# Performance work log

Hardware: AMD Instinct MI355X
Metric: run time of the kernel (lower is better)

Reference implementation:

```python
import jax, jax.numpy as jnp
import numpy as np

EPS = 1e-8
EPS12 = 1e-12
TAU = 0.2
IOU_THRESHOLD = 0.5
NEG_INF = -1e9

N, C = 8192, 1024
HID, FGD, CLSD = 256, 64, 128


def setup_inputs() -> dict:
    key = jax.random.key(0)
    ks = jax.random.split(key, 16)
    roi_feats = jax.random.normal(ks[0], (N, C), dtype=jnp.float32)
    # labels in {-1 (ignore), 0 (bg), 1..20 (classes)}
    labels = jax.random.randint(ks[1], (N,), 0, 21, dtype=jnp.int64) - 1
    ious = jax.random.uniform(ks[2], (N,), dtype=jnp.float32)
    s = 0.02
    w1f = jax.random.normal(ks[3], (HID, C), dtype=jnp.float32) * s
    b1f = jnp.zeros((HID,), dtype=jnp.float32)
    w2f = jax.random.normal(ks[4], (FGD, HID), dtype=jnp.float32) * s
    b2f = jnp.zeros((FGD,), dtype=jnp.float32)
    w1c = jax.random.normal(ks[5], (HID, C), dtype=jnp.float32) * s
    b1c = jnp.zeros((HID,), dtype=jnp.float32)
    w2c = jax.random.normal(ks[6], (CLSD, HID), dtype=jnp.float32) * s
    b2c = jnp.zeros((CLSD,), dtype=jnp.float32)
    return {"roi_feats": roi_feats, "labels": labels, "ious": ious,
            "w1f": w1f, "b1f": b1f, "w2f": w2f, "b2f": b2f,
            "w1c": w1c, "b1c": b1c, "w2c": w2c, "b2c": b2c}


def _project_normalize(x, w1, b1, w2, b2):
    h = jax.nn.relu(x @ w1.T + b1)
    z = h @ w2.T + b2
    nrm = jnp.linalg.norm(z, axis=1, keepdims=True)  # F.normalize: z / max(||z||, eps)
    return z / jnp.maximum(nrm, EPS)


def _fg_bg_loss(z_fg, fg_mask, ignore_mask, iou_weight):
    n = z_fg.shape[0]
    anchor = fg_mask & ~ignore_mask
    eye = jnp.eye(n, dtype=bool)
    # pos_mask[i,j] = fg_mask[j] & ~ignore[j], self excluded
    pos = (fg_mask & ~ignore_mask)[None, :] & ~eye  # [N,N]
    sim = (z_fg @ z_fg.T) / TAU
    sim_exp = jnp.exp(sim) * (~eye).astype(sim.dtype)
    denom = sim_exp.sum(axis=1)  # [N]
    numer = jnp.sum(jnp.exp(sim) * pos.astype(sim.dtype), axis=1)  # [N]
    n_pos = pos.sum(axis=1)
    loss_i = -jnp.log((numer + EPS) / (denom + EPS))
    valid = anchor & (n_pos > 0)
    w = iou_weight
    num = jnp.sum(jnp.where(valid, loss_i * w, 0.0))
    den = jnp.sum(jnp.where(valid, w, 0.0)) + EPS
    return num / den


def _class_supcon_loss(z_cls, labels, fg_mask, ignore_mask, iou_weight):
    n = z_cls.shape[0]
    anchor = fg_mask & ~ignore_mask
    eye = jnp.eye(n, dtype=bool)
    valid_den = ~eye & ~ignore_mask[None, :]  # [N,N]
    # pos[i,j]: same label, j not ignored, labels[j] != 0, j != i, j valid
    pos = (labels[None, :] == labels[:, None]) & ~ignore_mask[None, :] & (labels[None, :] != 0)
    pos = pos & ~eye & valid_den
    sim = (z_cls @ z_cls.T) / TAU
    logits = jnp.where(valid_den, sim, NEG_INF)
    denom_log = jax.nn.logsumexp(logits, axis=1)  # [N]
    n_pos = pos.sum(axis=1)
    sum_pos = jnp.sum(jnp.where(pos, sim, 0.0), axis=1)
    n_pos_safe = jnp.maximum(n_pos, 1).astype(sim.dtype)
    loss_i = -(sum_pos - n_pos.astype(sim.dtype) * denom_log) / n_pos_safe
    valid = anchor & (n_pos > 0) & valid_den.any(axis=1)
    w = iou_weight
    num = jnp.sum(jnp.where(valid, loss_i * w, 0.0))
    den = jnp.sum(jnp.where(valid, w, 0.0)) + EPS12
    return num / den


def reference(roi_feats, labels, ious, w1f, b1f, w2f, b2f, w1c, b1c, w2c, b2c):
    z_fg = _project_normalize(roi_feats, w1f, b1f, w2f, b2f)
    z_cls = _project_normalize(roi_feats, w1c, b1c, w2c, b2c)
    ignore_mask = labels == -1
    bg_mask = (labels == 0) & ~ignore_mask
    fg_mask = (labels > 0) & ~ignore_mask
    iou_weight = jnp.where(ious > IOU_THRESHOLD, ious, 0.0)
    loss_fg_bg = _fg_bg_loss(z_fg, fg_mask, ignore_mask, iou_weight)
    loss_supcon = _class_supcon_loss(z_cls, labels, fg_mask, ignore_mask, iou_weight)
    # loss_weights = (1.0, 1.0); stacked as [loss_fg_bg, loss_supcon]
    return jnp.stack([loss_fg_bg * 1.0, loss_supcon * 1.0])
```

## Files before the change

### kernel.cpp

```cpp
#include <hip/hip_runtime.h>
#include <hip/hip_bf16.h>
#include <math.h>

#define N_ROI 8192
#define C_IN  1024
#define HIDD  256
#define FGD   64
#define CLSD  128
#define INV_TAU 5.0f
#define SCALE_LOG2E 7.2134752f
#define LN2F 0.69314718f

using frag_ab = __attribute__((ext_vector_type(8))) short;
using f32x16  = __attribute__((ext_vector_type(16))) float;

static __device__ __forceinline__ short f32_to_bf16_bits(float f) {
  unsigned u = __builtin_bit_cast(unsigned, f);
  u = (u + 0x7FFFu + ((u >> 16) & 1u)) >> 16;
  return (short)u;
}
static __device__ __forceinline__ float bf16_bits_to_f32(short b) {
  unsigned u = ((unsigned)(unsigned short)b) << 16;
  return __builtin_bit_cast(float, u);
}
static __device__ __forceinline__ float fast_exp2(float x) {
#if __has_builtin(__builtin_amdgcn_exp2f)
  return __builtin_amdgcn_exp2f(x);
#else
  return exp2f(x);
#endif
}
static __device__ __forceinline__ void async_copy16(const void* g, void* l) {
  __builtin_amdgcn_global_load_lds(
      (const __attribute__((address_space(1))) unsigned int*)g,
      (__attribute__((address_space(3))) unsigned int*)l, 16, 0, 0);
}

__global__ __launch_bounds__(256) void pack_zero_kernel(
    const float* __restrict__ w1f, const float* __restrict__ w1c,
    const float* __restrict__ w2f, const float* __restrict__ w2c,
    short* __restrict__ W1pf, short* __restrict__ W1pc,
    short* __restrict__ W2pf, short* __restrict__ W2pc,
    float* __restrict__ accum, int* __restrict__ cnt) {
  int b = blockIdx.x;
  if (b == 280) {
    int t = threadIdx.x;
    if (t < 8) accum[t] = 0.f;
    if (t < 24) cnt[t] = 0;
    return;
  }
  const float* src; short* dst; int Ksh; int b0;
  if (b < 128)      { src = w1f; dst = W1pf; Ksh = 10; b0 = 0; }
  else if (b < 256) { src = w1c; dst = W1pc; Ksh = 10; b0 = 128; }
  else if (b < 264) { src = w2f; dst = W2pf; Ksh = 8;  b0 = 256; }
  else              { src = w2c; dst = W2pc; Ksh = 8;  b0 = 264; }
  int K = 1 << Ksh;
  int f = (b - b0) * 256 + threadIdx.x;
  int r = f >> (Ksh - 3);
  int c0 = (f & ((K >> 3) - 1)) << 3;
  float4 v0 = *(const float4*)(src + (size_t)r * K + c0);
  float4 v1 = *(const float4*)(src + (size_t)r * K + c0 + 4);
  union { short s[8]; uint4 v; } o;
  o.s[0] = f32_to_bf16_bits(v0.x); o.s[1] = f32_to_bf16_bits(v0.y);
  o.s[2] = f32_to_bf16_bits(v0.z); o.s[3] = f32_to_bf16_bits(v0.w);
  o.s[4] = f32_to_bf16_bits(v1.x); o.s[5] = f32_to_bf16_bits(v1.y);
  o.s[6] = f32_to_bf16_bits(v1.z); o.s[7] = f32_to_bf16_bits(v1.w);
  ((uint4*)dst)[(size_t)((r >> 5) * (K >> 4) + (c0 >> 4)) * 64 +
                ((c0 >> 3) & 1) * 32 + (r & 31)] = o.v;
}

template<int D>
__device__ __forceinline__ void gemm2_from_lds(
    const short* __restrict__ T2,
    const short* __restrict__ W2p, const float* __restrict__ b2,
    short* __restrict__ Zr, float* __restrict__ tii,
    short* __restrict__ T, int gt) {
  int lane = threadIdx.x & 63;
  const frag_ab* Wv = (const frag_ab*)W2p;
  constexpr int NT = D / 32;
  frag_ab a[16];
  #pragma unroll
  for (int kc = 0; kc < 16; ++kc)
    a[kc] = *(const frag_ab*)&T2[(lane & 31) * 264 + kc * 16 + (lane >> 5) * 8];
  f32x16 acc[NT];
  #pragma unroll
  for (int j = 0; j < NT; ++j)
    #pragma unroll
    for (int q = 0; q < 16; ++q) acc[j][q] = 0.f;
  #pragma unroll
  for (int kc = 0; kc < 16; ++kc)
    #pragma unroll
    for (int j = 0; j < NT; ++j)
      acc[j] = __builtin_amdgcn_mfma_f32_32x32x16_bf16(a[kc], Wv[(j * 16 + kc) * 64 + lane], acc[j], 0, 0, 0);
  int c = lane & 31, h = lane >> 5;
  float bb[NT];
  #pragma unroll
  for (int j = 0; j < NT; ++j) bb[j] = b2[j * 32 + c];
  float s1[16];
  #pragma unroll
  for (int r = 0; r < 16; ++r) {
    s1[r] = 0.f;
    #pragma unroll
    for (int j = 0; j < NT; ++j) {
      float v = acc[j][r] + bb[j];
      s1[r] += v * v;
    }
  }
  #pragma unroll
  for (int r = 0; r < 16; ++r)
    #pragma unroll
    for (int m = 1; m < 32; m <<= 1) s1[r] += __shfl_xor(s1[r], m);
  float s2[16];
  #pragma unroll
  for (int r = 0; r < 16; ++r) s2[r] = 0.f;
  #pragma unroll
  for (int j = 0; j < NT; ++j) {
    int cl = j * 32 + c;
    #pragma unroll
    for (int g = 0; g < 4; ++g) {
      short q0, q1, q2, q3;
      #pragma unroll
      for (int e = 0; e < 4; ++e) {
        int r = g * 4 + e;
        float sc = 1.f / fmaxf(sqrtf(s1[r]), 1e-8f);
        short qb = f32_to_bf16_bits((acc[j][r] + bb[j]) * sc);
        float zf = bf16_bits_to_f32(qb);
        s2[r] += zf * zf;
        if (e == 0) q0 = qb; else if (e == 1) q1 = qb; else if (e == 2) q2 = qb; else q3 = qb;
      }
      *(short4*)&T[cl * 36 + 4 * h + 8 * g] = make_short4(q0, q1, q2, q3);
    }
  }
  #pragma unroll
  for (int r = 0; r < 16; ++r)
    #pragma unroll
    for (int m = 1; m < 32; m <<= 1) s2[r] += __shfl_xor(s2[r], m);
  if (c == 0) {
    #pragma unroll
    for (int r = 0; r < 16; ++r)
      tii[gt * 32 + (r & 3) + 8 * (r >> 2) + 4 * h] = s2[r];
  }
  uint4* Zv = (uint4*)Zr;
  #pragma unroll
  for (int k = 0; k < D / 16; ++k) {
    int c0 = (2 * k + h) * 8;
    union { short s[8]; uint4 u; } o;
    #pragma unroll
    for (int e = 0; e < 8; ++e) o.s[e] = T[(c0 + e) * 36 + c];
    Zv[(size_t)(gt * (D / 16) + k) * 64 + h * 32 + c] = o.u;
  }
}

__global__ __launch_bounds__(256) void fused_mlp_kernel(
    const float* __restrict__ X,
    const short* __restrict__ W1pf, const short* __restrict__ W1pc,
    const float* __restrict__ b1f, const float* __restrict__ b1c,
    const short* __restrict__ W2pf, const short* __restrict__ W2pc,
    const float* __restrict__ b2f, const float* __restrict__ b2c,
    short* __restrict__ Zrf, short* __restrict__ Zrc,
    float* __restrict__ tiif, float* __restrict__ tiic,
    const int* __restrict__ labels,
    float* __restrict__ Sfg, float* __restrict__ Pfg,
    float* __restrict__ Scls, float* __restrict__ SPc,
    float* __restrict__ pfv, float* __restrict__ nimv,
    float* __restrict__ ljmv, int* __restrict__ cnt) {
  __shared__ short stageA[2][1024];
  __shared__ short T2[32 * 264];
  __shared__ short Tw[128 * 36];
  int tid = threadIdx.x, lane = tid & 63, wv = tid >> 6;
  int Mb = blockIdx.x, head = blockIdx.y;

  if (head == 0 && tid < 32) {
    int i = Mb * 32 + tid;
    Sfg[i] = 0.f; Pfg[i] = 0.f; Scls[i] = 0.f; SPc[i] = 0.f;
    int l = labels[i];
    pfv[i]  = (l > 0)  ? 1.f : 0.f;
    nimv[i] = (l != -1) ? 1.f : 0.f;
    ljmv[i] = (l > 0)  ? (float)l : -7.f;
    int b = l + 1; if (b < 0) b = 0; if (b > 21) b = 21;
    atomicAdd(&cnt[b], 1);
  }

  const short* Wp = head ? W1pc : W1pf;
  const float* b1 = head ? b1c  : b1f;
  const uint4* Wv4 = (const uint4*)Wp;
  int arow = tid >> 3;
  int ac4  = tid & 7;
  const float* Xp = X + (size_t)(Mb * 32 + arow) * C_IN + ac4 * 4;
  int aslot = ((ac4 >> 2) * 64 + ((ac4 >> 1) & 1) * 32 + arow) * 8 + (ac4 & 1) * 4;

  float4 av[4];
  frag_ab breg[3][4];
  f32x16 acc[2];
  #pragma unroll
  for (int nt = 0; nt < 2; ++nt)
    #pragma unroll
    for (int q = 0; q < 16; ++q) acc[nt][q] = 0.f;

  auto loadA = [&](int c, int s) { av[s] = *(const float4*)(Xp + c * 32); };
  auto loadB = [&](int c, int s) {
    #pragma unroll
    for (int kci = 0; kci < 2; ++kci)
      #pragma unroll
      for (int nt = 0; nt < 2; ++nt)
        breg[s][kci * 2 + nt] =
            *(const frag_ab*)&Wv4[(size_t)((wv * 2 + nt) * 64 + c * 2 + kci) * 64 + lane];
  };
  auto storeA = [&](int buf, int s) {
    *(short4*)&stageA[buf][aslot] =
        make_short4(f32_to_bf16_bits(av[s].x), f32_to_bf16_bits(av[s].y),
                    f32_to_bf16_bits(av[s].z), f32_to_bf16_bits(av[s].w));
  };
  auto domfma = [&](int buf, int bank) {
    frag_ab a0 = *(const frag_ab*)&stageA[buf][(0 * 64 + lane) * 8];
    frag_ab a1 = *(const frag_ab*)&stageA[buf][(1 * 64 + lane) * 8];
    #pragma unroll
    for (int nt = 0; nt < 2; ++nt)
      acc[nt] = __builtin_amdgcn_mfma_f32_32x32x16_bf16(a0, breg[bank][nt], acc[nt], 0, 0, 0);
    #pragma unroll
    for (int nt = 0; nt < 2; ++nt)
      acc[nt] = __builtin_amdgcn_mfma_f32_32x32x16_bf16(a1, breg[bank][2 + nt], acc[nt], 0, 0, 0);
  };
  auto lds_barrier = [&]() {
    asm volatile("s_waitcnt lgkmcnt(0)" ::: "memory");
    __builtin_amdgcn_s_barrier();
    __builtin_amdgcn_sched_barrier(0);
  };

  loadA(0, 0); loadA(1, 1); loadA(2, 2); loadA(3, 3);
  loadB(0, 0); loadB(1, 1);
  storeA(0, 0);
  lds_barrier();

  #pragma unroll
  for (int c = 0; c < 32; ++c) {
    if (c + 2 < 32) loadB(c + 2, (c + 2) % 3);
    if (c + 4 < 32) loadA(c + 4, (c + 4) & 3);
    domfma(c & 1, c % 3);
    if (c + 1 < 32) {
      storeA((c + 1) & 1, (c + 1) & 3);
      lds_barrier();
    }
  }
  {
    int cl31 = lane & 31, h = lane >> 5;
    #pragma unroll
    for (int nt = 0; nt < 2; ++nt) {
      int gc = wv * 64 + nt * 32 + cl31;
      float bb = b1[gc];
      #pragma unroll
      for (int q = 0; q < 16; ++q) {
        int row = (q & 3) + 8 * (q >> 2) + 4 * h;
        float x = fmaxf(acc[nt][q] + bb, 0.f);
        T2[row * 264 + gc] = f32_to_bf16_bits(x);
      }
    }
  }
  __syncthreads();

  if (wv == 0) {
    if (head == 0)
      gemm2_from_lds<FGD>(T2, W2pf, b2f, Zrf, tiif, Tw, Mb);
    else
      gemm2_from_lds<CLSD>(T2, W2pc, b2c, Zrc, tiic, Tw, Mb);
  }
}

template<int D, int MODE, int NJT>
__device__ __forceinline__ void loss_body(
    const short* __restrict__ Zr, const int* __restrict__ labels,
    const float* __restrict__ pfv, const float* __restrict__ nimv,
    const float* __restrict__ ljmv,
    float* __restrict__ Sg, float* __restrict__ Pg,
    short* __restrict__ smem) {
  constexpr int KC = D / 16;
  constexpr int JP = (MODE == 0) ? 2 : 1;
  constexpr int NIT = NJT / JP;
  constexpr int BUF_SH = 4096;
  int tid = threadIdx.x, lane = tid & 63, wv = tid >> 6;
  int itile = (blockIdx.x >> 1) * 8 + wv;
  int jt0 = blockIdx.y * NJT;
  int jlane = lane & 31;
  const frag_ab* Zrv = (const frag_ab*)Zr;

  frag_ab a[KC];
  #pragma unroll
  for (int kc = 0; kc < KC; ++kc) {
    frag_ab t = Zrv[(itile * KC + kc) * 64 + lane];
    #pragma unroll
    for (int e = 0; e < 8; ++e)
      t[e] = f32_to_bf16_bits(bf16_bits_to_f32(t[e]) * SCALE_LOG2E);
    a[kc] = t;
  }
  float limf[16];
  if (MODE == 1) {
    #pragma unroll
    for (int r = 0; r < 16; ++r) {
      int row = (r & 3) + 8 * (r >> 2) + 4 * (lane >> 5);
      limf[r] = (float)labels[itile * 32 + row];
    }
  }
  __builtin_amdgcn_sched_barrier(0);
  asm volatile("s_waitcnt vmcnt(0)" ::: "memory");
  __builtin_amdgcn_sched_barrier(0);

  short* b0 = smem;
  short* b1 = smem + BUF_SH;
  short* b2 = smem + 2 * BUF_SH;
  float* maskf = (float*)(smem + 3 * BUF_SH);

  if (MODE == 0) {
    async_copy16(pfv + jt0 * 32 + (size_t)(tid & 127) * 4,
                 maskf + (wv & 1) * 256);
  } else {
    const float* msrc = ((wv & 2) == 0) ? nimv : ljmv;
    float* mdst = maskf + ((wv & 2) ? 512 : 0) + (wv & 1) * 256;
    async_copy16(msrc + jt0 * 32 + (size_t)(tid & 127) * 4, mdst);
  }

  auto STAGE = [&](short* dst, int it) {
    const short* src = Zr + (size_t)(jt0 + it * JP) * KC * 512 / JP * JP;
    async_copy16(src + (size_t)tid * 8, dst + wv * 512);
  };

  STAGE(b0, 0); STAGE(b1, 1);

  float Ssum[16] = {}, Psum[16] = {};

  #pragma unroll 1
  for (int t = 0; t < NIT; ++t) {
    if (t < NIT - 1) asm volatile("s_waitcnt vmcnt(1)" ::: "memory");
    else             asm volatile("s_waitcnt vmcnt(0)" ::: "memory");
    __builtin_amdgcn_s_barrier();
    __builtin_amdgcn_sched_barrier(0);
    if (t + 2 < NIT) STAGE(b2, t + 2);

    if (MODE == 0) {
      float pf0 = maskf[t * 64 + jlane];
      float pf1 = maskf[t * 64 + 32 + jlane];
      f32x16 acc0, acc1;
      #pragma unroll
      for (int q = 0; q < 16; ++q) { acc0[q] = 0.f; acc1[q] = 0.f; }
      __builtin_amdgcn_s_setprio(1);
      #pragma unroll
      for (int kc = 0; kc < KC; ++kc) {
        frag_ab bb0 = *(const frag_ab*)&b0[(kc * 64 + lane) * 8];
        frag_ab bb1 = *(const frag_ab*)&b0[((KC + kc) * 64 + lane) * 8];
        acc0 = __builtin_amdgcn_mfma_f32_32x32x16_bf16(a[kc], bb0, acc0, 0, 0, 0);
        acc1 = __builtin_amdgcn_mfma_f32_32x32x16_bf16(a[kc], bb1, acc1, 0, 0, 0);
      }
      __builtin_amdgcn_s_setprio(0);
      #pragma unroll
      for (int rr = 0; rr < 16; ++rr) {
        float e0 = fast_exp2(acc0[rr]);
        float e1 = fast_exp2(acc1[rr]);
        Ssum[rr] += e0 + e1;
        Psum[rr] = fmaf(pf0, e0, fmaf(pf1, e1, Psum[rr]));
      }
    } else {
      float nim = maskf[t * 32 + jlane];
      float ljm = maskf[512 + t * 32 + jlane];
      f32x16 acc;
      #pragma unroll
      for (int q = 0; q < 16; ++q) acc[q] = 0.f;
      __builtin_amdgcn_s_setprio(1);
      #pragma unroll
      for (int kc = 0; kc < KC; ++kc) {
        frag_ab b = *(const frag_ab*)&b0[(kc * 64 + lane) * 8];
        acc = __builtin_amdgcn_mfma_f32_32x32x16_bf16(a[kc], b, acc, 0, 0, 0);
      }
      __builtin_amdgcn_s_setprio(0);
      #pragma unroll
      for (int rr = 0; rr < 16; ++rr) {
        float e = fast_exp2(acc[rr]);
        Ssum[rr] = fmaf(nim, e, Ssum[rr]);
        Psum[rr] += (limf[rr] == ljm) ? acc[rr] : 0.f;
      }
    }
    short* tmp = b0; b0 = b1; b1 = b2; b2 = tmp;
  }

  #pragma unroll
  for (int r = 0; r < 16; ++r) {
    float s = Ssum[r], p = Psum[r];
    #pragma unroll
    for (int m = 1; m < 32; m <<= 1) { s += __shfl_xor(s, m); p += __shfl_xor(p, m); }
    if ((lane & 31) == 0) {
      if (MODE == 1) p *= LN2F;
      int row = (r & 3) + 8 * (r >> 2) + 4 * (lane >> 5);
      atomicAdd(&Sg[itile * 32 + row], s);
      atomicAdd(&Pg[itile * 32 + row], p);
    }
  }
}

__global__ __launch_bounds__(512, 2) void loss_kernel(
    const short* __restrict__ Zrf, const short* __restrict__ Zrc,
    const int* __restrict__ labels,
    const float* __restrict__ pfv, const float* __restrict__ nimv,
    const float* __restrict__ ljmv,
    float* __restrict__ Sfg, float* __restrict__ Pfg,
    float* __restrict__ Scls, float* __restrict__ SPc) {
  __shared__ short smem[3 * 4096 + 2048];
  if ((blockIdx.x & 1) == 0)
    loss_body<FGD, 0, 16>(Zrf, labels, pfv, nimv, ljmv, Sfg, Pfg, smem);
  else
    loss_body<CLSD, 1, 16>(Zrc, labels, pfv, nimv, ljmv, Scls, SPc, smem);
}

__global__ __launch_bounds__(256) void finalize_kernel(
    const float* __restrict__ Sfg, const float* __restrict__ Pfg,
    const float* __restrict__ Scls, const float* __restrict__ SPc,
    const float* __restrict__ tiif, const float* __restrict__ tiic,
    const int* __restrict__ labels, const float* __restrict__ ious,
    int* __restrict__ cnt, float* __restrict__ accum, float* __restrict__ out) {
  int i = blockIdx.x * 256 + threadIdx.x;
  int l = labels[i];
  float iv = ious[i];
  float w = (iv > 0.5f) ? iv : 0.f;
  int cntP = 0;
  #pragma unroll
  for (int b = 2; b <= 21; ++b) cntP += cnt[b];
  int cntNI = N_ROI - cnt[0];
  bool Pi = (l > 0);
  float numF = 0.f, denF = 0.f, numC = 0.f, denC = 0.f;
  float eF = __expf(INV_TAU * tiif[i]);
  float Sf = Sfg[i] - eF;
  float Pf = Pfg[i] - (Pi ? eF : 0.f);
  int nposF = cntP - (Pi ? 1 : 0);
  if (Pi && nposF > 0) {
    float lossF = logf((Sf + 1e-8f) / (Pf + 1e-8f));
    numF = lossF * w; denF = w;
  }
  float tC = INV_TAU * tiic[i];
  float eC = __expf(tC);
  float Sc = Scls[i] - ((l != -1) ? eC : 0.f);
  float SP = SPc[i] - (Pi ? tC : 0.f);
  int nposC = Pi ? (cnt[l + 1] - 1) : 0;
  bool anyv = (cntNI - ((l != -1) ? 1 : 0)) > 0;
  if (Pi && nposC > 0 && anyv) {
    float lse = logf(Sc);
    float lossC = -(SP - (float)nposC * lse) / fmaxf((float)nposC, 1.f);
    numC = lossC * w; denC = w;
  }
  float v0 = numF, v1 = denF, v2 = numC, v3 = denC;
  #pragma unroll
  for (int m = 1; m < 64; m <<= 1) {
    v0 += __shfl_xor(v0, m); v1 += __shfl_xor(v1, m);
    v2 += __shfl_xor(v2, m); v3 += __shfl_xor(v3, m);
  }
  __shared__ float red[4][4];
  int lane = threadIdx.x & 63, wid = threadIdx.x >> 6;
  if (lane == 0) { red[wid][0]=v0; red[wid][1]=v1; red[wid][2]=v2; red[wid][3]=v3; }
  __syncthreads();
  if (threadIdx.x == 0) {
    float s0=0,s1=0,s2=0,s3=0;
    for (int q = 0; q < 4; ++q) { s0+=red[q][0]; s1+=red[q][1]; s2+=red[q][2]; s3+=red[q][3]; }
    atomicAdd(&accum[0], s0); atomicAdd(&accum[1], s1);
    atomicAdd(&accum[2], s2); atomicAdd(&accum[3], s3);
    __threadfence();
    int t = atomicAdd(&cnt[22], 1);
    if (t == 31) {
      __threadfence();
      out[0] = accum[0] / (accum[1] + 1e-8f);
      out[1] = accum[2] / (accum[3] + 1e-12f);
    }
  }
}

extern "C" void kernel_launch(void* const* d_in, const int* in_sizes, int n_in,
                              void* d_out, int out_size, void* d_ws, size_t ws_size,
                              hipStream_t stream) {
  const float* X    = (const float*)d_in[0];
  const int*  labels= (const int*)d_in[1];
  const float* ious = (const float*)d_in[2];
  const float* w1f  = (const float*)d_in[3];
  const float* b1f  = (const float*)d_in[4];
  const float* w2f  = (const float*)d_in[5];
  const float* b2f  = (const float*)d_in[6];
  const float* w1c  = (const float*)d_in[7];
  const float* b1c  = (const float*)d_in[8];
  const float* w2c  = (const float*)d_in[9];
  const float* b2c  = (const float*)d_in[10];
  float* out = (float*)d_out;

  char* w = (char*)d_ws;
  short* W1pf = (short*)w;            w += 524288;
  short* W1pc = (short*)w;            w += 524288;
  short* W2pf = (short*)w;            w += 32768;
  short* W2pc = (short*)w;            w += 65536;
  short* Zrf  = (short*)w;            w += 1048576;
  short* Zrc  = (short*)w;            w += 2097152;
  float* Sfg  = (float*)w;            w += 32768;
  float* Pfg  = (float*)w;            w += 32768;
  float* Scls = (float*)w;            w += 32768;
  float* SPc  = (float*)w;            w += 32768;
  float* tiif = (float*)w;            w += 32768;
  float* tiic = (float*)w;            w += 32768;
  float* pfv  = (float*)w;            w += 32768;
  float* nimv = (float*)w;            w += 32768;
  float* ljmv = (float*)w;            w += 32768;
  float* accum= (float*)w;            w += 32;
  int*   cnt  = (int*)w;              w += 96;

  pack_zero_kernel<<<281, 256, 0, stream>>>(w1f, w1c, w2f, w2c,
                                            W1pf, W1pc, W2pf, W2pc, accum, cnt);

  fused_mlp_kernel<<<dim3(256, 2), 256, 0, stream>>>(X, W1pf, W1pc, b1f, b1c,
                                            W2pf, W2pc, b2f, b2c,
                                            Zrf, Zrc, tiif, tiic,
                                            labels, Sfg, Pfg, Scls, SPc,
                                            pfv, nimv, ljmv, cnt);

  loss_kernel<<<dim3(64, 16), 512, 0, stream>>>(Zrf, Zrc, labels, pfv, nimv, ljmv,
                                                Sfg, Pfg, Scls, SPc);

  finalize_kernel<<<N_ROI/256, 256, 0, stream>>>(Sfg, Pfg, Scls, SPc, tiif, tiic,
                                                 labels, ious, cnt, accum, out);
}
```

Measured before the change: 184.9 us.

## Replace per-pair positive-sim sum with per-class embedding sums and dot product

The same-class positive similarity sum is rewritten algebraically as z_i dotted with the sum of z_j over class l_i. A new kernel builds the 20 per-class sums, and the finalize kernel computes the dot product, so the class loss loop no longer needs label compares or a second accumulator. The class branch now processes two j-tiles per iteration like the fg branch, with larger LDS buffers. This adds a kernel launch and atomics, and the dot product uses unscaled bf16 Z, which may shift precision slightly.

```diff
diff --git a/kernel.cpp b/kernel.cpp
--- a/kernel.cpp
+++ b/kernel.cpp
@@ -41,12 +41,14 @@
     const float* __restrict__ w2f, const float* __restrict__ w2c,
     short* __restrict__ W1pf, short* __restrict__ W1pc,
     short* __restrict__ W2pf, short* __restrict__ W2pc,
-    float* __restrict__ accum, int* __restrict__ cnt) {
+    float* __restrict__ accum, int* __restrict__ cnt,
+    float* __restrict__ Vc) {
   int b = blockIdx.x;
   if (b == 280) {
     int t = threadIdx.x;
     if (t < 8) accum[t] = 0.f;
     if (t < 24) cnt[t] = 0;
+    for (int q = t; q < 2560; q += 256) Vc[q] = 0.f;
     return;
   }
   const float* src; short* dst; int Ksh; int b0;
@@ -161,9 +163,9 @@
     float* __restrict__ tiif, float* __restrict__ tiic,
     const int* __restrict__ labels,
     float* __restrict__ Sfg, float* __restrict__ Pfg,
-    float* __restrict__ Scls, float* __restrict__ SPc,
+    float* __restrict__ Scls,
     float* __restrict__ pfv, float* __restrict__ nimv,
-    float* __restrict__ ljmv, int* __restrict__ cnt) {
+    int* __restrict__ cnt) {
   __shared__ short stageA[2][1024];
   __shared__ short T2[32 * 264];
   __shared__ short Tw[128 * 36];
@@ -172,11 +174,10 @@
 
   if (head == 0 && tid < 32) {
     int i = Mb * 32 + tid;
-    Sfg[i] = 0.f; Pfg[i] = 0.f; Scls[i] = 0.f; SPc[i] = 0.f;
+    Sfg[i] = 0.f; Pfg[i] = 0.f; Scls[i] = 0.f;
     int l = labels[i];
     pfv[i]  = (l > 0)  ? 1.f : 0.f;
     nimv[i] = (l != -1) ? 1.f : 0.f;
-    ljmv[i] = (l > 0)  ? (float)l : -7.f;
     int b = l + 1; if (b < 0) b = 0; if (b > 21) b = 21;
     atomicAdd(&cnt[b], 1);
   }
@@ -266,17 +267,48 @@
   }
 }
 
+__global__ __launch_bounds__(128) void classsum_kernel(
+    const short* __restrict__ Zrc, const int* __restrict__ labels,
+    float* __restrict__ Vc) {
+  __shared__ int lidx[512];
+  __shared__ int lcnt;
+  int c = blockIdx.x + 1;
+  int d = threadIdx.x;
+  int j0 = blockIdx.y * 512;
+  if (d == 0) lcnt = 0;
+  __syncthreads();
+  #pragma unroll
+  for (int u = 0; u < 4; ++u) {
+    int row = j0 + u * 128 + d;
+    if (labels[row] == c) {
+      int k = atomicAdd(&lcnt, 1);
+      lidx[k] = row;
+    }
+  }
+  __syncthreads();
+  int n = lcnt;
+  int kc = d >> 4, h = (d >> 3) & 1, e = d & 7;
+  float acc = 0.f;
+  for (int k = 0; k < n; ++k) {
+    int row = lidx[k];
+    int jt = row >> 5, r = row & 31;
+    acc += bf16_bits_to_f32(
+        Zrc[((size_t)((jt * 8 + kc) * 64 + h * 32 + r)) * 8 + e]);
+  }
+  atomicAdd(&Vc[(c - 1) * 128 + d], acc);
+}
+
 template<int D, int MODE, int NJT>
 __device__ __forceinline__ void loss_body(
-    const short* __restrict__ Zr, const int* __restrict__ labels,
-    const float* __restrict__ pfv, const float* __restrict__ nimv,
-    const float* __restrict__ ljmv,
+    const short* __restrict__ Zr,
+    const float* __restrict__ maskv,
     float* __restrict__ Sg, float* __restrict__ Pg,
     short* __restrict__ smem) {
   constexpr int KC = D / 16;
-  constexpr int JP = (MODE == 0) ? 2 : 1;
+  constexpr int JP = 2;
   constexpr int NIT = NJT / JP;
-  constexpr int BUF_SH = 4096;
+  constexpr int BUFQ = JP * KC * 512;
+  constexpr int LD = BUFQ / 4096;
   int tid = threadIdx.x, lane = tid & 63, wv = tid >> 6;
   int itile = (blockIdx.x >> 1) * 8 + wv;
   int jt0 = blockIdx.y * NJT;
@@ -292,35 +324,23 @@
       t[e] = f32_to_bf16_bits(bf16_bits_to_f32(t[e]) * SCALE_LOG2E);
     a[kc] = t;
   }
-  float limf[16];
-  if (MODE == 1) {
-    #pragma unroll
-    for (int r = 0; r < 16; ++r) {
-      int row = (r & 3) + 8 * (r >> 2) + 4 * (lane >> 5);
-      limf[r] = (float)labels[itile * 32 + row];
-    }
-  }
   __builtin_amdgcn_sched_barrier(0);
   asm volatile("s_waitcnt vmcnt(0)" ::: "memory");
   __builtin_amdgcn_sched_barrier(0);
 
   short* b0 = smem;
-  short* b1 = smem + BUF_SH;
-  short* b2 = smem + 2 * BUF_SH;
-  float* maskf = (float*)(smem + 3 * BUF_SH);
-
-  if (MODE == 0) {
-    async_copy16(pfv + jt0 * 32 + (size_t)(tid & 127) * 4,
-                 maskf + (wv & 1) * 256);
-  } else {
-    const float* msrc = ((wv & 2) == 0) ? nimv : ljmv;
-    float* mdst = maskf + ((wv & 2) ? 512 : 0) + (wv & 1) * 256;
-    async_copy16(msrc + jt0 * 32 + (size_t)(tid & 127) * 4, mdst);
-  }
+  short* b1 = smem + BUFQ;
+  short* b2 = smem + 2 * BUFQ;
+  float* maskf = (float*)(smem + 3 * BUFQ);
+
+  async_copy16(maskv + jt0 * 32 + (size_t)(tid & 127) * 4,
+               maskf + (wv & 1) * 256);
 
   auto STAGE = [&](short* dst, int it) {
-    const short* src = Zr + (size_t)(jt0 + it * JP) * KC * 512 / JP * JP;
-    async_copy16(src + (size_t)tid * 8, dst + wv * 512);
+    const short* src = Zr + (size_t)(jt0 + it * JP) * KC * 512;
+    #pragma unroll
+    for (int u = 0; u < LD; ++u)
+      async_copy16(src + (size_t)(u * 512 + tid) * 8, dst + u * 4096 + wv * 512);
   };
 
   STAGE(b0, 0); STAGE(b1, 1);
@@ -329,52 +349,37 @@
 
   #pragma unroll 1
   for (int t = 0; t < NIT; ++t) {
-    if (t < NIT - 1) asm volatile("s_waitcnt vmcnt(1)" ::: "memory");
-    else             asm volatile("s_waitcnt vmcnt(0)" ::: "memory");
+    if (t < NIT - 1) {
+      if constexpr (LD == 1) asm volatile("s_waitcnt vmcnt(1)" ::: "memory");
+      else                   asm volatile("s_waitcnt vmcnt(2)" ::: "memory");
+    } else {
+      asm volatile("s_waitcnt vmcnt(0)" ::: "memory");
+    }
     __builtin_amdgcn_s_barrier();
     __builtin_amdgcn_sched_barrier(0);
     if (t + 2 < NIT) STAGE(b2, t + 2);
 
-    if (MODE == 0) {
-      float pf0 = maskf[t * 64 + jlane];
-      float pf1 = maskf[t * 64 + 32 + jlane];
-      f32x16 acc0, acc1;
-      #pragma unroll
-      for (int q = 0; q < 16; ++q) { acc0[q] = 0.f; acc1[q] = 0.f; }
-      __builtin_amdgcn_s_setprio(1);
-      #pragma unroll
-      for (int kc = 0; kc < KC; ++kc) {
-        frag_ab bb0 = *(const frag_ab*)&b0[(kc * 64 + lane) * 8];
-        frag_ab bb1 = *(const frag_ab*)&b0[((KC + kc) * 64 + lane) * 8];
-        acc0 = __builtin_amdgcn_mfma_f32_32x32x16_bf16(a[kc], bb0, acc0, 0, 0, 0);
-        acc1 = __builtin_amdgcn_mfma_f32_32x32x16_bf16(a[kc], bb1, acc1, 0, 0, 0);
-      }
-      __builtin_amdgcn_s_setprio(0);
-      #pragma unroll
-      for (int rr = 0; rr < 16; ++rr) {
-        float e0 = fast_exp2(acc0[rr]);
-        float e1 = fast_exp2(acc1[rr]);
+    float m0 = maskf[t * 64 + jlane];
+    float m1 = maskf[t * 64 + 32 + jlane];
+    f32x16 acc0, acc1;
+    #pragma unroll
+    for (int q = 0; q < 16; ++q) { acc0[q] = 0.f; acc1[q] = 0.f; }
+    #pragma unroll
+    for (int kc = 0; kc < KC; ++kc) {
+      frag_ab bb0 = *(const frag_ab*)&b0[(kc * 64 + lane) * 8];
+      frag_ab bb1 = *(const frag_ab*)&b0[((KC + kc) * 64 + lane) * 8];
+      acc0 = __builtin_amdgcn_mfma_f32_32x32x16_bf16(a[kc], bb0, acc0, 0, 0, 0);
+      acc1 = __builtin_amdgcn_mfma_f32_32x32x16_bf16(a[kc], bb1, acc1, 0, 0, 0);
+    }
+    #pragma unroll
+    for (int rr = 0; rr < 16; ++rr) {
+      float e0 = fast_exp2(acc0[rr]);
+      float e1 = fast_exp2(acc1[rr]);
+      if (MODE == 0) {
         Ssum[rr] += e0 + e1;
-        Psum[rr] = fmaf(pf0, e0, fmaf(pf1, e1, Psum[rr]));
-      }
-    } else {
-      float nim = maskf[t * 32 + jlane];
-      float ljm = maskf[512 + t * 32 + jlane];
-      f32x16 acc;
-      #pragma unroll
-      for (int q = 0; q < 16; ++q) acc[q] = 0.f;
-      __builtin_amdgcn_s_setprio(1);
-      #pragma unroll
-      for (int kc = 0; kc < KC; ++kc) {
-        frag_ab b = *(const frag_ab*)&b0[(kc * 64 + lane) * 8];
-        acc = __builtin_amdgcn_mfma_f32_32x32x16_bf16(a[kc], b, acc, 0, 0, 0);
-      }
-      __builtin_amdgcn_s_setprio(0);
-      #pragma unroll
-      for (int rr = 0; rr < 16; ++rr) {
-        float e = fast_exp2(acc[rr]);
-        Ssum[rr] = fmaf(nim, e, Ssum[rr]);
-        Psum[rr] += (limf[rr] == ljm) ? acc[rr] : 0.f;
+        Psum[rr] = fmaf(m0, e0, fmaf(m1, e1, Psum[rr]));
+      } else {
+        Ssum[rr] = fmaf(m1, e1, fmaf(m0, e0, Ssum[rr]));
       }
     }
     short* tmp = b0; b0 = b1; b1 = b2; b2 = tmp;
@@ -384,33 +389,34 @@
   for (int r = 0; r < 16; ++r) {
     float s = Ssum[r], p = Psum[r];
     #pragma unroll
-    for (int m = 1; m < 32; m <<= 1) { s += __shfl_xor(s, m); p += __shfl_xor(p, m); }
+    for (int m = 1; m < 32; m <<= 1) {
+      s += __shfl_xor(s, m);
+      if (MODE == 0) p += __shfl_xor(p, m);
+    }
     if ((lane & 31) == 0) {
-      if (MODE == 1) p *= LN2F;
       int row = (r & 3) + 8 * (r >> 2) + 4 * (lane >> 5);
       atomicAdd(&Sg[itile * 32 + row], s);
-      atomicAdd(&Pg[itile * 32 + row], p);
+      if (MODE == 0) atomicAdd(&Pg[itile * 32 + row], p);
     }
   }
 }
 
 __global__ __launch_bounds__(512, 2) void loss_kernel(
     const short* __restrict__ Zrf, const short* __restrict__ Zrc,
-    const int* __restrict__ labels,
     const float* __restrict__ pfv, const float* __restrict__ nimv,
-    const float* __restrict__ ljmv,
     float* __restrict__ Sfg, float* __restrict__ Pfg,
-    float* __restrict__ Scls, float* __restrict__ SPc) {
-  __shared__ short smem[3 * 4096 + 2048];
+    float* __restrict__ Scls) {
+  __shared__ short smem[3 * 8192 + 1024];
   if ((blockIdx.x & 1) == 0)
-    loss_body<FGD, 0, 16>(Zrf, labels, pfv, nimv, ljmv, Sfg, Pfg, smem);
+    loss_body<FGD, 0, 16>(Zrf, pfv, Sfg, Pfg, smem);
   else
-    loss_body<CLSD, 1, 16>(Zrc, labels, pfv, nimv, ljmv, Scls, SPc, smem);
+    loss_body<CLSD, 1, 16>(Zrc, nimv, Scls, nullptr, smem);
 }
 
 __global__ __launch_bounds__(256) void finalize_kernel(
     const float* __restrict__ Sfg, const float* __restrict__ Pfg,
-    const float* __restrict__ Scls, const float* __restrict__ SPc,
+    const float* __restrict__ Scls,
+    const short* __restrict__ Zrc, const float* __restrict__ Vc,
     const float* __restrict__ tiif, const float* __restrict__ tiic,
     const int* __restrict__ labels, const float* __restrict__ ious,
     int* __restrict__ cnt, float* __restrict__ accum, float* __restrict__ out) {
@@ -435,7 +441,21 @@
   float tC = INV_TAU * tiic[i];
   float eC = __expf(tC);
   float Sc = Scls[i] - ((l != -1) ? eC : 0.f);
-  float SP = SPc[i] - (Pi ? tC : 0.f);
+  float SPdot = 0.f;
+  if (Pi) {
+    const float* V = Vc + (size_t)(l - 1) * 128;
+    int jt = i >> 5, r = i & 31;
+    #pragma unroll
+    for (int kc = 0; kc < 8; ++kc)
+      #pragma unroll
+      for (int h = 0; h < 2; ++h) {
+        frag_ab z = *(const frag_ab*)&Zrc[((size_t)((jt * 8 + kc) * 64 + h * 32 + r)) * 8];
+        #pragma unroll
+        for (int e = 0; e < 8; ++e)
+          SPdot += bf16_bits_to_f32(z[e]) * V[kc * 16 + h * 8 + e];
+      }
+  }
+  float SP = SPdot * INV_TAU - (Pi ? tC : 0.f);
   int nposC = Pi ? (cnt[l + 1] - 1) : 0;
   bool anyv = (cntNI - ((l != -1) ? 1 : 0)) > 0;
   if (Pi && nposC > 0 && anyv) {
@@ -502,19 +522,24 @@
   float* ljmv = (float*)w;            w += 32768;
   float* accum= (float*)w;            w += 32;
   int*   cnt  = (int*)w;              w += 96;
+  float* Vc   = (float*)w;            w += 10240;
+  (void)SPc; (void)ljmv;
 
   pack_zero_kernel<<<281, 256, 0, stream>>>(w1f, w1c, w2f, w2c,
-                                            W1pf, W1pc, W2pf, W2pc, accum, cnt);
+                                            W1pf, W1pc, W2pf, W2pc, accum, cnt, Vc);
 
   fused_mlp_kernel<<<dim3(256, 2), 256, 0, stream>>>(X, W1pf, W1pc, b1f, b1c,
                                             W2pf, W2pc, b2f, b2c,
                                             Zrf, Zrc, tiif, tiic,
-                                            labels, Sfg, Pfg, Scls, SPc,
-                                            pfv, nimv, ljmv, cnt);
-
-  loss_kernel<<<dim3(64, 16), 512, 0, stream>>>(Zrf, Zrc, labels, pfv, nimv, ljmv,
-                                                Sfg, Pfg, Scls, SPc);
-
-  finalize_kernel<<<N_ROI/256, 256, 0, stream>>>(Sfg, Pfg, Scls, SPc, tiif, tiic,
+                                            labels, Sfg, Pfg, Scls,
+                                            pfv, nimv, cnt);
+
+  classsum_kernel<<<dim3(20, 16), 128, 0, stream>>>(Zrc, labels, Vc);
+
+  loss_kernel<<<dim3(64, 16), 512, 0, stream>>>(Zrf, Zrc, pfv, nimv,
+                                                Sfg, Pfg, Scls);
+
+  finalize_kernel<<<N_ROI/256, 256, 0, stream>>>(Sfg, Pfg, Scls, Zrc, Vc,
+                                                 tiif, tiic,
                                                  labels, ious, cnt, accum, out);
 }
```

Measured after the change: 184.3 us. About the same (-0.3%).
